# Kernel tuning notes

Measured on AMD Instinct MI355X. Metric: run time of the kernel, lower is better.

Reference implementation:

```python
import jax, jax.numpy as jnp
import numpy as np

N, K, D = 32768, 8192, 256


def setup_inputs() -> dict:
    key = jax.random.key(0)
    k1, k2 = jax.random.split(key)
    x = jax.random.normal(k1, (N, D), dtype=jnp.float32)
    vectors = jax.random.normal(k2, (K, D), dtype=jnp.float32)  # codebook
    return {"x": x, "vectors": vectors}


def reference(x, vectors):
    # torch.cdist(x[:,None,:], vectors[None]) followed by argmin over K.
    # Euclidean distance is monotone in squared distance, so argmin over the
    # without a sqrt, matching the original math exactly for the returned ids.
    x2 = jnp.sum(x * x, axis=-1, keepdims=True)          # [N, 1]
    c2 = jnp.sum(vectors * vectors, axis=-1)             # [K]
    d2 = x2 + c2 - 2.0 * jnp.matmul(x, vectors.T)        # [N, K]
    indices = jnp.argmin(d2, axis=-1)                    # [N]
    return indices.astype(jnp.int32)
```

## Files before the change

kernel.cpp:

```cpp
#include <hip/hip_runtime.h>
#include <stdint.h>
#include <stddef.h>


#define N_PTS 32768
#define K_CB  8192
#define D_DIM 256
#define TM 128
#define TN 128
#define SPLITK 4
#define KCHUNK (K_CB / SPLITK)
#define NTILES (KCHUNK / TN)
#define NCHUNKS (NTILES * 8)

#define WS_XH   0
#define WS_XL   (WS_XH + N_PTS * D_DIM * 2)
#define WS_CH   (WS_XL + N_PTS * D_DIM * 2)
#define WS_CL   (WS_CH + K_CB * D_DIM * 2)
#define WS_C2   (WS_CL + K_CB * D_DIM * 2)
#define WS_PD   (WS_C2 + K_CB * 4)
#define WS_PI   (WS_PD + SPLITK * N_PTS * 4)
#define WS_END  (WS_PI + SPLITK * N_PTS * 4)

typedef _Float16 half4v __attribute__((ext_vector_type(4)));
typedef _Float16 half8v __attribute__((ext_vector_type(8)));
typedef float    f32x4  __attribute__((ext_vector_type(4)));

__device__ __forceinline__ void gld16(const void* g, void* l) {
    __builtin_amdgcn_global_load_lds(
        (const __attribute__((address_space(1))) void*)g,
        (__attribute__((address_space(3))) void*)l, 16, 0, 0);
}


#define XBLOCKS (N_PTS * D_DIM / 4 / 256)
#define CBLOCKS (K_CB * D_DIM / 4 / 256)

__global__ void __launch_bounds__(256)
prep_kernel(const float* __restrict__ x, const float* __restrict__ vecs,
            _Float16* __restrict__ xh, _Float16* __restrict__ xl,
            _Float16* __restrict__ ch, _Float16* __restrict__ cl,
            float* __restrict__ c2) {
    const int b = blockIdx.x;
    if (b < XBLOCKS) {
        const int i = b * 256 + threadIdx.x;
        const float4 v = ((const float4*)x)[i];
        half4v h = {(_Float16)v.x, (_Float16)v.y, (_Float16)v.z, (_Float16)v.w};
        half4v l = {(_Float16)((v.x - (float)h[0]) * 2048.0f),
                    (_Float16)((v.y - (float)h[1]) * 2048.0f),
                    (_Float16)((v.z - (float)h[2]) * 2048.0f),
                    (_Float16)((v.w - (float)h[3]) * 2048.0f)};
        *(half4v*)(xh + (size_t)i * 4) = h;
        *(half4v*)(xl + (size_t)i * 4) = l;
    } else {
        const int i = (b - XBLOCKS) * 256 + threadIdx.x;
        const float4 v = ((const float4*)vecs)[i];
        half4v h = {(_Float16)v.x, (_Float16)v.y, (_Float16)v.z, (_Float16)v.w};
        half4v l = {(_Float16)((v.x - (float)h[0]) * 2048.0f),
                    (_Float16)((v.y - (float)h[1]) * 2048.0f),
                    (_Float16)((v.z - (float)h[2]) * 2048.0f),
                    (_Float16)((v.w - (float)h[3]) * 2048.0f)};
        *(half4v*)(ch + (size_t)i * 4) = h;
        *(half4v*)(cl + (size_t)i * 4) = l;
        float s = v.x * v.x + v.y * v.y + v.z * v.z + v.w * v.w;
#pragma unroll
        for (int off = 32; off > 0; off >>= 1) s += __shfl_down(s, off, 64);
        if ((threadIdx.x & 63) == 0) c2[i >> 6] = s;
    }
}

__global__ void __launch_bounds__(256)
cnorms_kernel(const float* __restrict__ vecs, float* __restrict__ c2) {
    int gwave = (blockIdx.x * 256 + threadIdx.x) >> 6;
    int lane  = threadIdx.x & 63;
    const float* src = vecs + (size_t)gwave * D_DIM;
    float4 v = ((const float4*)src)[lane];
    float s = v.x * v.x + v.y * v.y + v.z * v.z + v.w * v.w;
#pragma unroll
    for (int off = 32; off > 0; off >>= 1) s += __shfl_down(s, off, 64);
    if (lane == 0) c2[gwave] = s;
}


__global__ void __launch_bounds__(256, 2)
vq_main_fast(const _Float16* __restrict__ xh_g, const _Float16* __restrict__ xl_g,
             const _Float16* __restrict__ ch_g, const _Float16* __restrict__ cl_g,
             const float* __restrict__ c2, float* __restrict__ pd, int* __restrict__ pi) {
    __shared__ __align__(16) char lds[65536];

    const int t    = threadIdx.x;
    const int lane = t & 63;
    const int wv   = t >> 6;
    const int wy   = wv >> 1, wx = wv & 1;
    const int fr   = lane & 15;
    const int g    = lane >> 4;

    const int split = blockIdx.x & (SPLITK - 1);
    const int pbase = (blockIdx.x >> 2) * TM;
    const int kbase = split * KCHUNK;

    const int srowoff = (lane >> 2) * (D_DIM * 2)
                      + ((((lane & 3) ^ ((lane >> 3) & 3))) << 4);
    const char* xh_s = (const char*)xh_g + (size_t)(pbase + wv * 32) * (D_DIM * 2) + srowoff;
    const char* xl_s = (const char*)xl_g + (size_t)(pbase + wv * 32) * (D_DIM * 2) + srowoff;
    const char* ch_s = (const char*)ch_g + (size_t)(kbase + wv * 32) * (D_DIM * 2) + srowoff;
    const char* cl_s = (const char*)cl_g + (size_t)(kbase + wv * 32) * (D_DIM * 2) + srowoff;
    const int stA = wv * 2048;

    const int skey = (fr >> 1) & 3;
    int aoff[4], boff[4];
#pragma unroll
    for (int i = 0; i < 4; ++i) {
        aoff[i] = (wy * 64 + i * 16 + fr) * 64 + ((g ^ skey) << 4);
        boff[i] = 16384 + (wx * 64 + i * 16 + fr) * 64 + ((g ^ skey) << 4);
    }

    f32x4 acc[4][4];

    auto STAGE = [&](char* L, int c) {
        const size_t kofs = (size_t)(c >> 3) * (TN * D_DIM * 2);
        const int gofs = (c & 7) * 64;
#pragma unroll
        for (int q = 0; q < 2; ++q) {
            gld16(xh_s + q * 8192 + gofs, L +         stA + q * 1024);
            gld16(xl_s + q * 8192 + gofs, L +  8192 + stA + q * 1024);
            gld16(ch_s + kofs + q * 8192 + gofs, L + 16384 + stA + q * 1024);
            gld16(cl_s + kofs + q * 8192 + gofs, L + 24576 + stA + q * 1024);
        }
    };

    auto COMPUTE = [&](const char* L) {
        half8v a1[4], a2[4], a3[4];
#pragma unroll
        for (int i = 0; i < 4; ++i) {
            const char* p = L + aoff[i];
            a1[i] = *(const half8v*)p;
            a3[i] = *(const half8v*)(p + 8192);
            a2[i] = a1[i] * (_Float16)4.8828125e-4f;
        }
#pragma unroll
        for (int j = 0; j < 4; ++j) {
            const char* p = L + boff[j];
            half8v b1 = *(const half8v*)p;
            half8v b2 = *(const half8v*)(p + 8192);
            half8v b3 = b1 * (_Float16)4.8828125e-4f;
#pragma unroll
            for (int i = 0; i < 4; ++i) {
                acc[i][j] = __builtin_amdgcn_mfma_f32_16x16x32_f16(a1[i], b1, acc[i][j], 0, 0, 0);
                acc[i][j] = __builtin_amdgcn_mfma_f32_16x16x32_f16(a2[i], b2, acc[i][j], 0, 0, 0);
                acc[i][j] = __builtin_amdgcn_mfma_f32_16x16x32_f16(a3[i], b3, acc[i][j], 0, 0, 0);
            }
        }
    };

    float best[16];
    int   bidx[16];
#pragma unroll
    for (int i = 0; i < 16; ++i) { best[i] = 3.4e38f; bidx[i] = 0; }

    STAGE(lds, 0);

#pragma unroll 1
    for (int kt = 0; kt < NTILES; ++kt) {
#pragma unroll
        for (int i = 0; i < 4; ++i)
#pragma unroll
            for (int j = 0; j < 4; ++j) {
                f32x4 z = {0.f, 0.f, 0.f, 0.f};
                acc[i][j] = z;
            }

#pragma unroll 1
        for (int dkc = 0; dkc < 8; ++dkc) {
            const int c = kt * 8 + dkc;
            if (c + 1 < NCHUNKS) {
                STAGE(lds + (((c + 1) & 1) << 15), c + 1);
                asm volatile("s_waitcnt vmcnt(8)" ::: "memory");
            } else {
                asm volatile("s_waitcnt vmcnt(0)" ::: "memory");
            }
            __builtin_amdgcn_sched_barrier(0);
            __builtin_amdgcn_s_barrier();
            __builtin_amdgcn_sched_barrier(0);
            COMPUTE(lds + ((c & 1) << 15));
            __builtin_amdgcn_sched_barrier(0);
            __builtin_amdgcn_s_barrier();
        }

        const int ktbase = kbase + kt * TN;
#pragma unroll
        for (int j = 0; j < 4; ++j) {
            const int cg = ktbase + wx * 64 + j * 16 + fr;
            const float c2v = c2[cg];
#pragma unroll
            for (int i = 0; i < 4; ++i)
#pragma unroll
                for (int r = 0; r < 4; ++r) {
                    const float v = fmaf(-2.0f, acc[i][j][r], c2v);
                    const int s = i * 4 + r;
                    if (v < best[s]) { best[s] = v; bidx[s] = cg; }
                }
        }
    }

    __syncthreads();
    float* rd = (float*)lds;
    int*   ri = (int*)lds + 256;
#pragma unroll
    for (int i = 0; i < 4; ++i)
#pragma unroll
        for (int r = 0; r < 4; ++r) {
            float bv = best[i * 4 + r];
            int   bi = bidx[i * 4 + r];
#pragma unroll
            for (int off = 1; off < 16; off <<= 1) {
                const float ov = __shfl_xor(bv, off, 64);
                const int   oi = __shfl_xor(bi, off, 64);
                if (ov < bv || (ov == bv && oi < bi)) { bv = ov; bi = oi; }
            }
            if (fr == 0) {
                const int rowl = wy * 64 + i * 16 + g * 4 + r;
                rd[rowl * 2 + wx] = bv;
                ri[rowl * 2 + wx] = bi;
            }
        }
    __syncthreads();
    if (t < TM) {
        float b0 = rd[t * 2];
        int   i0 = ri[t * 2];
        const float b1 = rd[t * 2 + 1];
        const int   i1 = ri[t * 2 + 1];
        if (b1 < b0 || (b1 == b0 && i1 < i0)) { b0 = b1; i0 = i1; }
        pd[split * N_PTS + pbase + t] = b0;
        pi[split * N_PTS + pbase + t] = i0;
    }
}


#define BK 32
#define LS (BK + 4)

__device__ inline half8v load8(const _Float16* p) {
    half4v a = *(const half4v*)p;
    half4v b = *(const half4v*)(p + 4);
    return __builtin_shufflevector(a, b, 0, 1, 2, 3, 4, 5, 6, 7);
}

struct Trip { _Float16 h, s2, l2; };

__device__ inline Trip cvt3(float v) {
    Trip t;
    _Float16 hh = (_Float16)v;
    float hf = (float)hh;
    t.h  = hh;
    t.s2 = (_Float16)(hf * 4.8828125e-4f);
    t.l2 = (_Float16)((v - hf) * 2048.0f);
    return t;
}

__global__ void __launch_bounds__(256, 2)
vq_main_v3(const float* __restrict__ x, const float* __restrict__ vecs,
           const float* __restrict__ c2, float* __restrict__ pd, int* __restrict__ pi) {
    __shared__ _Float16 lds[6 * TM * LS];
    _Float16* xh  = lds;
    _Float16* xs2 = lds + 1 * TM * LS;
    _Float16* xl2 = lds + 2 * TM * LS;
    _Float16* ch  = lds + 3 * TM * LS;
    _Float16* cl2 = lds + 4 * TM * LS;
    _Float16* cs2 = lds + 5 * TM * LS;

    const int t     = threadIdx.x;
    const int split = blockIdx.x & (SPLITK - 1);
    const int pbase = (blockIdx.x >> 2) * TM;
    const int kbase = split * KCHUNK;

    const int lane = t & 63;
    const int wv   = t >> 6;
    const int wy   = wv >> 1, wx = wv & 1;
    const int fr   = lane & 15;
    const int g    = lane >> 4;
    const int kb   = g * 8;

    const int srow = t >> 3;
    const int sc4  = (t & 7) * 4;

    float best[16];
    int   bidx[16];
#pragma unroll
    for (int i = 0; i < 16; ++i) { best[i] = 3.4e38f; bidx[i] = 0; }

    for (int kt = 0; kt < NTILES; ++kt) {
        const int ktbase = kbase + kt * TN;
        f32x4 acc[4][4];
#pragma unroll
        for (int i = 0; i < 4; ++i)
#pragma unroll
            for (int j = 0; j < 4; ++j) {
                f32x4 z = {0.f, 0.f, 0.f, 0.f};
                acc[i][j] = z;
            }
        for (int dk = 0; dk < D_DIM; dk += BK) {
            __syncthreads();
#pragma unroll
            for (int p = 0; p < 4; ++p) {
                const int row = srow + p * 32;
                const float4 v = *(const float4*)&x[(size_t)(pbase + row) * D_DIM + dk + sc4];
                const Trip t0 = cvt3(v.x), t1 = cvt3(v.y), t2 = cvt3(v.z), t3 = cvt3(v.w);
                half4v h  = {t0.h,  t1.h,  t2.h,  t3.h};
                half4v s2 = {t0.s2, t1.s2, t2.s2, t3.s2};
                half4v l2 = {t0.l2, t1.l2, t2.l2, t3.l2};
                *(half4v*)&xh [row * LS + sc4] = h;
                *(half4v*)&xs2[row * LS + sc4] = s2;
                *(half4v*)&xl2[row * LS + sc4] = l2;
                const float4 w = *(const float4*)&vecs[(size_t)(ktbase + row) * D_DIM + dk + sc4];
                const Trip u0 = cvt3(w.x), u1 = cvt3(w.y), u2 = cvt3(w.z), u3 = cvt3(w.w);
                half4v hc = {u0.h,  u1.h,  u2.h,  u3.h};
                half4v sc = {u0.s2, u1.s2, u2.s2, u3.s2};
                half4v lc = {u0.l2, u1.l2, u2.l2, u3.l2};
                *(half4v*)&ch [row * LS + sc4] = hc;
                *(half4v*)&cs2[row * LS + sc4] = sc;
                *(half4v*)&cl2[row * LS + sc4] = lc;
            }
            __syncthreads();
            half8v a1[4], a2[4], a3[4], b1[4], b2[4], b3[4];
#pragma unroll
            for (int i = 0; i < 4; ++i) {
                const int aoff = (wy * 64 + i * 16 + fr) * LS + kb;
                a1[i] = load8(&xh [aoff]);
                a2[i] = load8(&xs2[aoff]);
                a3[i] = load8(&xl2[aoff]);
                const int boff2 = (wx * 64 + i * 16 + fr) * LS + kb;
                b1[i] = load8(&ch [boff2]);
                b2[i] = load8(&cl2[boff2]);
                b3[i] = load8(&cs2[boff2]);
            }
#pragma unroll
            for (int i = 0; i < 4; ++i)
#pragma unroll
                for (int j = 0; j < 4; ++j) {
                    acc[i][j] = __builtin_amdgcn_mfma_f32_16x16x32_f16(a1[i], b1[j], acc[i][j], 0, 0, 0);
                    acc[i][j] = __builtin_amdgcn_mfma_f32_16x16x32_f16(a2[i], b2[j], acc[i][j], 0, 0, 0);
                    acc[i][j] = __builtin_amdgcn_mfma_f32_16x16x32_f16(a3[i], b3[j], acc[i][j], 0, 0, 0);
                }
        }
#pragma unroll
        for (int j = 0; j < 4; ++j) {
            const int cg = ktbase + wx * 64 + j * 16 + fr;
            const float c2v = c2[cg];
#pragma unroll
            for (int i = 0; i < 4; ++i)
#pragma unroll
                for (int r = 0; r < 4; ++r) {
                    const float v = fmaf(-2.0f, acc[i][j][r], c2v);
                    const int s = i * 4 + r;
                    if (v < best[s]) { best[s] = v; bidx[s] = cg; }
                }
        }
    }
    __syncthreads();
    float* rd = (float*)lds;
    int*   ri = (int*)lds + 256;
#pragma unroll
    for (int i = 0; i < 4; ++i)
#pragma unroll
        for (int r = 0; r < 4; ++r) {
            float bv = best[i * 4 + r];
            int   bi = bidx[i * 4 + r];
#pragma unroll
            for (int off = 1; off < 16; off <<= 1) {
                const float ov = __shfl_xor(bv, off, 64);
                const int   oi = __shfl_xor(bi, off, 64);
                if (ov < bv || (ov == bv && oi < bi)) { bv = ov; bi = oi; }
            }
            if (fr == 0) {
                const int rowl = wy * 64 + i * 16 + g * 4 + r;
                rd[rowl * 2 + wx] = bv;
                ri[rowl * 2 + wx] = bi;
            }
        }
    __syncthreads();
    if (t < TM) {
        float b0 = rd[t * 2];
        int   i0 = ri[t * 2];
        const float b1 = rd[t * 2 + 1];
        const int   i1 = ri[t * 2 + 1];
        if (b1 < b0 || (b1 == b0 && i1 < i0)) { b0 = b1; i0 = i1; }
        pd[split * N_PTS + pbase + t] = b0;
        pi[split * N_PTS + pbase + t] = i0;
    }
}


__global__ void __launch_bounds__(256)
vq_combine(const float* __restrict__ pd, const int* __restrict__ pi,
           int* __restrict__ out) {
    const int p = blockIdx.x * 256 + threadIdx.x;
    float bb = pd[p];
    int   bi = pi[p];
#pragma unroll
    for (int s = 1; s < SPLITK; ++s) {
        const float v  = pd[s * N_PTS + p];
        const int   vi = pi[s * N_PTS + p];
        if (v < bb || (v == bb && vi < bi)) { bb = v; bi = vi; }
    }
    out[p] = bi;
}

extern "C" void kernel_launch(void* const* d_in, const int* in_sizes, int n_in,
                              void* d_out, int out_size, void* d_ws, size_t ws_size,
                              hipStream_t stream) {
    const float* x    = (const float*)d_in[0];
    const float* vecs = (const float*)d_in[1];
    int* out = (int*)d_out;
    char* ws = (char*)d_ws;

    if (ws_size >= (size_t)WS_END) {
        _Float16* xh = (_Float16*)(ws + WS_XH);
        _Float16* xl = (_Float16*)(ws + WS_XL);
        _Float16* ch = (_Float16*)(ws + WS_CH);
        _Float16* cl = (_Float16*)(ws + WS_CL);
        float* c2 = (float*)(ws + WS_C2);
        float* pd = (float*)(ws + WS_PD);
        int*   pi = (int*)(ws + WS_PI);

        hipLaunchKernelGGL(prep_kernel, dim3(XBLOCKS + CBLOCKS), dim3(256), 0, stream,
                           x, vecs, xh, xl, ch, cl, c2);
        hipLaunchKernelGGL(vq_main_fast, dim3((N_PTS / TM) * SPLITK), dim3(256), 0, stream,
                           xh, xl, ch, cl, c2, pd, pi);
        hipLaunchKernelGGL(vq_combine, dim3(N_PTS / 256), dim3(256), 0, stream,
                           pd, pi, out);
    } else {
        float* c2 = (float*)ws;
        float* pd = (float*)ws + K_CB;
        int*   pi = (int*)((float*)ws + K_CB + SPLITK * N_PTS);
        hipLaunchKernelGGL(cnorms_kernel, dim3(K_CB / 4), dim3(256), 0, stream,
                           vecs, c2);
        hipLaunchKernelGGL(vq_main_v3, dim3((N_PTS / TM) * SPLITK), dim3(256), 0, stream,
                           x, vecs, c2, pd, pi);
        hipLaunchKernelGGL(vq_combine, dim3(N_PTS / 256), dim3(256), 0, stream,
                           pd, pi, out);
    }
}
```

Before: 480.9 us.

## Load X fragments directly to registers from pre-tiled layout; triple-buffer codebook in LDS

The prep kernel now writes the hi/lo fp16 split of x in a fragment-tiled layout, so each wave can load its MFMA A operands straight from global memory into registers. Only the codebook tiles are staged through LDS, now in a three-buffer ring with a single barrier per chunk. X fragments are double-buffered in registers, and s_setprio raises wave priority during the MFMA phase. This cuts LDS traffic and footprint (48KB instead of 64KB) and drops one barrier per chunk, in exchange for more VGPR pressure and uncoalesced-looking per-wave global loads of x that repeat once per K tile.

Measured after the change: 505.8 us. 5.2% more time.

```diff
diff --git a/kernel.cpp b/kernel.cpp
--- a/kernel.cpp
+++ b/kernel.cpp
@@ -50,8 +50,12 @@
                     (_Float16)((v.y - (float)h[1]) * 2048.0f),
                     (_Float16)((v.z - (float)h[2]) * 2048.0f),
                     (_Float16)((v.w - (float)h[3]) * 2048.0f)};
-        *(half4v*)(xh + (size_t)i * 4) = h;
-        *(half4v*)(xl + (size_t)i * 4) = l;
+        const int f   = i * 4;
+        const int row = f >> 8, k0 = f & 255;
+        const size_t pa = ((size_t)(row >> 6) * 8 + (k0 >> 5)) * 4096
+                        + (row & 63) * 64 + ((k0 >> 3) & 3) * 16 + (k0 & 7) * 2;
+        *(half4v*)((char*)xh + pa) = h;
+        *(half4v*)((char*)xl + pa) = l;
     } else {
         const int i = (b - XBLOCKS) * 256 + threadIdx.x;
         const float4 v = ((const float4*)vecs)[i];
@@ -83,10 +87,10 @@
 
 
 __global__ void __launch_bounds__(256, 2)
-vq_main_fast(const _Float16* __restrict__ xh_g, const _Float16* __restrict__ xl_g,
+vq_main_fast(const _Float16* __restrict__ xh_p, const _Float16* __restrict__ xl_p,
              const _Float16* __restrict__ ch_g, const _Float16* __restrict__ cl_g,
              const float* __restrict__ c2, float* __restrict__ pd, int* __restrict__ pi) {
-    __shared__ __align__(16) char lds[65536];
+    __shared__ __align__(16) char lds[49152];
 
     const int t    = threadIdx.x;
     const int lane = t & 63;
@@ -99,48 +103,53 @@
     const int pbase = (blockIdx.x >> 2) * TM;
     const int kbase = split * KCHUNK;
 
-    const int srowoff = (lane >> 2) * (D_DIM * 2)
+    const int srowoff = (lane >> 2) * 512
                       + ((((lane & 3) ^ ((lane >> 3) & 3))) << 4);
-    const char* xh_s = (const char*)xh_g + (size_t)(pbase + wv * 32) * (D_DIM * 2) + srowoff;
-    const char* xl_s = (const char*)xl_g + (size_t)(pbase + wv * 32) * (D_DIM * 2) + srowoff;
-    const char* ch_s = (const char*)ch_g + (size_t)(kbase + wv * 32) * (D_DIM * 2) + srowoff;
-    const char* cl_s = (const char*)cl_g + (size_t)(kbase + wv * 32) * (D_DIM * 2) + srowoff;
-    const int stA = wv * 2048;
+    const char* ch_s = (const char*)ch_g + (size_t)(kbase + wv * 32) * 512 + srowoff;
+    const char* cl_s = (const char*)cl_g + (size_t)(kbase + wv * 32) * 512 + srowoff;
+    const int stW = wv * 2048;
+
+    const int grp = (blockIdx.x >> 2) * 2 + wy;
+    const char* xhp = (const char*)xh_p + (size_t)grp * 32768 + fr * 64 + g * 16;
+    const char* xlp = (const char*)xl_p + (size_t)grp * 32768 + fr * 64 + g * 16;
 
     const int skey = (fr >> 1) & 3;
-    int aoff[4], boff[4];
-#pragma unroll
-    for (int i = 0; i < 4; ++i) {
-        aoff[i] = (wy * 64 + i * 16 + fr) * 64 + ((g ^ skey) << 4);
-        boff[i] = 16384 + (wx * 64 + i * 16 + fr) * 64 + ((g ^ skey) << 4);
-    }
+    int boff[4];
+#pragma unroll
+    for (int j = 0; j < 4; ++j)
+        boff[j] = (wx * 64 + j * 16 + fr) * 64 + ((g ^ skey) << 4);
 
     f32x4 acc[4][4];
-
-    auto STAGE = [&](char* L, int c) {
-        const size_t kofs = (size_t)(c >> 3) * (TN * D_DIM * 2);
+    half8v a1A[4], a3A[4], a1B[4], a3B[4];
+
+    auto STAGE = [&](int bw, int c) {
+        const size_t kofs = (size_t)(c >> 3) * (TN * 512);
         const int gofs = (c & 7) * 64;
-#pragma unroll
-        for (int q = 0; q < 2; ++q) {
-            gld16(xh_s + q * 8192 + gofs, L +         stA + q * 1024);
-            gld16(xl_s + q * 8192 + gofs, L +  8192 + stA + q * 1024);
-            gld16(ch_s + kofs + q * 8192 + gofs, L + 16384 + stA + q * 1024);
-            gld16(cl_s + kofs + q * 8192 + gofs, L + 24576 + stA + q * 1024);
-        }
+        char* B = lds + bw * 16384;
+        gld16(ch_s + kofs + gofs,        B +        stW);
+        gld16(ch_s + kofs + gofs + 8192, B +        stW + 1024);
+        gld16(cl_s + kofs + gofs,        B + 8192 + stW);
+        gld16(cl_s + kofs + gofs + 8192, B + 8192 + stW + 1024);
     };
 
-    auto COMPUTE = [&](const char* L) {
-        half8v a1[4], a2[4], a3[4];
+    auto XLOAD = [&](half8v* a1, half8v* a3, int c) {
+        const int xofs = (c & 7) * 4096;
 #pragma unroll
         for (int i = 0; i < 4; ++i) {
-            const char* p = L + aoff[i];
-            a1[i] = *(const half8v*)p;
-            a3[i] = *(const half8v*)(p + 8192);
+            a1[i] = *(const half8v*)(xhp + xofs + i * 1024);
+            a3[i] = *(const half8v*)(xlp + xofs + i * 1024);
+        }
+    };
+
+    auto COMPUTE = [&](int br, const half8v* a1, const half8v* a3) {
+        const char* B = lds + br * 16384;
+        half8v a2[4];
+#pragma unroll
+        for (int i = 0; i < 4; ++i)
             a2[i] = a1[i] * (_Float16)4.8828125e-4f;
-        }
 #pragma unroll
         for (int j = 0; j < 4; ++j) {
-            const char* p = L + boff[j];
+            const char* p = B + boff[j];
             half8v b1 = *(const half8v*)p;
             half8v b2 = *(const half8v*)(p + 8192);
             half8v b3 = b1 * (_Float16)4.8828125e-4f;
@@ -158,7 +167,9 @@
 #pragma unroll
     for (int i = 0; i < 16; ++i) { best[i] = 3.4e38f; bidx[i] = 0; }
 
-    STAGE(lds, 0);
+    STAGE(0, 0);
+    XLOAD(a1A, a3A, 0);
+    int br = 0;
 
 #pragma unroll 1
     for (int kt = 0; kt < NTILES; ++kt) {
@@ -171,20 +182,43 @@
             }
 
 #pragma unroll 1
-        for (int dkc = 0; dkc < 8; ++dkc) {
-            const int c = kt * 8 + dkc;
+        for (int du = 0; du < 4; ++du) {
+            int c = kt * 8 + du * 2;
+            int bw = (br == 2) ? 0 : br + 1;
             if (c + 1 < NCHUNKS) {
-                STAGE(lds + (((c + 1) & 1) << 15), c + 1);
-                asm volatile("s_waitcnt vmcnt(8)" ::: "memory");
+                STAGE(bw, c + 1);
+                XLOAD(a1B, a3B, c + 1);
+                __builtin_amdgcn_sched_barrier(0);
+                asm volatile("s_waitcnt vmcnt(12)" ::: "memory");
             } else {
+                __builtin_amdgcn_sched_barrier(0);
                 asm volatile("s_waitcnt vmcnt(0)" ::: "memory");
             }
             __builtin_amdgcn_sched_barrier(0);
             __builtin_amdgcn_s_barrier();
             __builtin_amdgcn_sched_barrier(0);
-            COMPUTE(lds + ((c & 1) << 15));
+            __builtin_amdgcn_s_setprio(1);
+            COMPUTE(br, a1A, a3A);
+            __builtin_amdgcn_s_setprio(0);
+            br = bw;
+            c = c + 1;
+            bw = (br == 2) ? 0 : br + 1;
+            if (c + 1 < NCHUNKS) {
+                STAGE(bw, c + 1);
+                XLOAD(a1A, a3A, c + 1);
+                __builtin_amdgcn_sched_barrier(0);
+                asm volatile("s_waitcnt vmcnt(12)" ::: "memory");
+            } else {
+                __builtin_amdgcn_sched_barrier(0);
+                asm volatile("s_waitcnt vmcnt(0)" ::: "memory");
+            }
             __builtin_amdgcn_sched_barrier(0);
             __builtin_amdgcn_s_barrier();
+            __builtin_amdgcn_sched_barrier(0);
+            __builtin_amdgcn_s_setprio(1);
+            COMPUTE(br, a1B, a3B);
+            __builtin_amdgcn_s_setprio(0);
+            br = bw;
         }
 
         const int ktbase = kbase + kt * TN;
```
